# Optimization experiments

Measured on AMD Instinct MI355X. Metric: run time of the kernel, lower is better.

The kernel has to match this reference:

```python
import jax, jax.numpy as jnp
import numpy as np

N = 50000      # nodes
E = 500000     # edges
D_IN = 64      # node_in_dim
K = 4          # edge_in_dim
H = 64         # node_hidden_dim
C = 40         # num_class
L = 2          # num_layers


def setup_inputs() -> dict:
    key = jax.random.key(0)
    ks = jax.random.split(key, 10)
    node_features = jax.random.normal(ks[0], (N, D_IN), jnp.float32)
    edge_features = jax.random.normal(ks[1], (L, E, K), jnp.float32)
    src = jax.random.randint(ks[2], (E,), 0, N)
    dst = jax.random.randint(ks[3], (E,), 0, N)
    W0 = jax.random.normal(ks[4], (K * D_IN, H), jnp.float32) * 0.05
    b0 = jnp.zeros((H,), jnp.float32)
    W1 = jax.random.normal(ks[5], (K * H, H), jnp.float32) * 0.05
    b1 = jnp.zeros((H,), jnp.float32)
    Wfc = jax.random.normal(ks[6], (H, C), jnp.float32) * 0.05
    bfc = jnp.zeros((C,), jnp.float32)
    return dict(node_features=node_features, edge_features=edge_features,
                src=src, dst=dst, W0=W0, b0=b0, W1=W1, b1=b1, Wfc=Wfc, bfc=bfc)


def reference(node_features, edge_features, src, dst, W0, b0, W1, b1, Wfc, bfc):
    h = node_features  # [N, d]
    ones = jnp.ones((E,), jnp.float32)
    cnt = jnp.maximum(jax.ops.segment_sum(ones, dst, num_segments=N), 1.0)  # in-degree
    for i, (W, b) in enumerate([(W0, b0), (W1, b1)]):
        e = edge_features[i]          # [E, K]
        hs = h[src]                   # [E, d] edge gather of src node features
        d = hs.shape[1]
        # message: relu(Linear(flatten(e[:,:,None] * h[:,None,:])))
        # flatten order is (K, d), so reshape W -> [K, d, H] and contract directly
        Wr = W.reshape(K, d, H)
        m = jax.nn.relu(jnp.einsum('ek,ed,kdh->eh', e, hs, Wr) + b)  # [E, H]
        s = jax.ops.segment_sum(m, dst, num_segments=N)              # scatter-sum
        h = jax.nn.relu(s / cnt[:, None])                            # mailbox mean + relu
    return h @ Wfc + bfc  # [N, C]
```

## Files before the change

### kernel.cpp

```cpp
#include <hip/hip_runtime.h>
#include <hip/hip_fp16.h>

#define N_NODES 50000
#define N_EDGES 500000
#define DIM 64
#define KDIM 4
#define HID 64
#define NCLS 40
#define NBLK ((N_NODES + 255) / 256)

__device__ inline unsigned pack2(float a, float b) {
    __half2 h = __floats2half2_rn(a, b);
    return *(unsigned*)&h;
}
__device__ inline float2 unpack2(unsigned u) {
    __half2 h = *(__half2*)&u;
    return __half22float2(h);
}

__global__ void hist_k(const int* __restrict__ dst, int* __restrict__ cnt) {
    int e = blockIdx.x * 256 + threadIdx.x;
    if (e < N_EDGES) atomicAdd(&cnt[dst[e]], 1);
}

__global__ __launch_bounds__(256) void scan_k(const int* __restrict__ cnt,
                                              int* __restrict__ start,
                                              int* __restrict__ cursor,
                                              volatile int* __restrict__ bflag,
                                              volatile int* __restrict__ bval) {
    __shared__ int ls[256];
    __shared__ int sbase;
    __shared__ int ok_all;
    int b = blockIdx.x, t = threadIdx.x;
    int n = b * 256 + t;
    int v = (n < N_NODES) ? cnt[n] : 0;
    ls[t] = v;
    __syncthreads();
#pragma unroll
    for (int off = 1; off < 256; off <<= 1) {
        int u = (t >= off) ? ls[t - off] : 0;
        __syncthreads();
        ls[t] += u;
        __syncthreads();
    }
    int incl = ls[t];
    int total = ls[255];
    __syncthreads();

    if (t == 0) {
        bval[b] = total;
        __threadfence();
        bflag[b] = 1;
    }

    if (b > 0) {
        for (;;) {
            int f = (t < b) ? bflag[t] : 1;
            if (t == 0) ok_all = 1;
            __syncthreads();
            if (!f) ok_all = 0;
            __syncthreads();
            if (ok_all) break;
        }
        __threadfence();
        int pv = (t < b) ? bval[t] : 0;
        ls[t] = pv;
        __syncthreads();
#pragma unroll
        for (int off = 128; off > 0; off >>= 1) {
            if (t < off) ls[t] += ls[t + off];
            __syncthreads();
        }
        if (t == 0) sbase = ls[0];
        __syncthreads();
    } else {
        if (t == 0) sbase = 0;
        __syncthreads();
    }

    int excl = sbase + incl - v;
    if (n < N_NODES) { start[n] = excl; cursor[n] = excl; }
    if (n == 0) start[N_NODES] = N_EDGES;
}

__global__ void scatter_k(const int* __restrict__ src, const int* __restrict__ dst,
                          const float* __restrict__ ef, int* __restrict__ cursor,
                          uint4* __restrict__ rec) {
    int e = blockIdx.x * 256 + threadIdx.x;
    if (e < N_EDGES) {
        int d = dst[e];
        int pos = atomicAdd(&cursor[d], 1);
        int sn = src[e];
        float4 f0 = ((const float4*)ef)[e];
        float4 f1 = ((const float4*)ef)[N_EDGES + e];
        rec[2 * pos]     = make_uint4((unsigned)sn, pack2(f0.x, f0.y), pack2(f0.z, f0.w), 0u);
        rec[2 * pos + 1] = make_uint4((unsigned)sn, pack2(f1.x, f1.y), pack2(f1.z, f1.w), 0u);
    }
}

__global__ __launch_bounds__(256) void transform_k(const float* __restrict__ hin,
                                                   const float* __restrict__ W,
                                                   unsigned* __restrict__ y) {
    __shared__ float sW[2 * 64 * 64];
    __shared__ float sh[64 * 65];
    int t = threadIdx.x;
    int kpair = blockIdx.y;

    const float4* W4 = (const float4*)(W + (size_t)kpair * 2 * 4096);
    float4* sW4 = (float4*)sW;
#pragma unroll
    for (int i = 0; i < 8; ++i) sW4[t + 256 * i] = W4[t + 256 * i];

    int n0 = blockIdx.x * 64;
#pragma unroll
    for (int i = 0; i < 4; ++i) {
        int idx = t + 256 * i;
        int nl = idx >> 4;
        int dg = idx & 15;
        int n = n0 + nl;
        float4 v = make_float4(0.f, 0.f, 0.f, 0.f);
        if (n < N_NODES) v = ((const float4*)hin)[(size_t)n * 16 + dg];
        sh[nl * 65 + dg * 4 + 0] = v.x;
        sh[nl * 65 + dg * 4 + 1] = v.y;
        sh[nl * 65 + dg * 4 + 2] = v.z;
        sh[nl * 65 + dg * 4 + 3] = v.w;
    }
    __syncthreads();

    int nl = t & 31;
    int cg = t >> 5;
    int k_local = cg >> 2;
    int hc0 = (cg & 3) * 16;

    float acc0[16], acc1[16];
#pragma unroll
    for (int j = 0; j < 16; ++j) { acc0[j] = 0.f; acc1[j] = 0.f; }

    for (int d = 0; d < 64; ++d) {
        float a0 = sh[nl * 65 + d];
        float a1 = sh[(nl + 32) * 65 + d];
        const float* wr = &sW[k_local * 4096 + d * 64 + hc0];
#pragma unroll
        for (int j = 0; j < 16; ++j) {
            float w = wr[j];
            acc0[j] = fmaf(a0, w, acc0[j]);
            acc1[j] = fmaf(a1, w, acc1[j]);
        }
    }

    int n_a = n0 + nl, n_b = n0 + nl + 32;
    int cbase = (kpair * 2 + k_local) * 64 + hc0;
    if (n_a < N_NODES) {
        uint4* o = (uint4*)(y + ((size_t)n_a * 256 + cbase) / 2);
        o[0] = make_uint4(pack2(acc0[0], acc0[1]), pack2(acc0[2], acc0[3]),
                          pack2(acc0[4], acc0[5]), pack2(acc0[6], acc0[7]));
        o[1] = make_uint4(pack2(acc0[8], acc0[9]), pack2(acc0[10], acc0[11]),
                          pack2(acc0[12], acc0[13]), pack2(acc0[14], acc0[15]));
    }
    if (n_b < N_NODES) {
        uint4* o = (uint4*)(y + ((size_t)n_b * 256 + cbase) / 2);
        o[0] = make_uint4(pack2(acc1[0], acc1[1]), pack2(acc1[2], acc1[3]),
                          pack2(acc1[4], acc1[5]), pack2(acc1[6], acc1[7]));
        o[1] = make_uint4(pack2(acc1[8], acc1[9]), pack2(acc1[10], acc1[11]),
                          pack2(acc1[12], acc1[13]), pack2(acc1[14], acc1[15]));
    }
}

__device__ inline void load_edge(const uint4 r, const unsigned* __restrict__ y,
                                 int lane, uint2& q0, uint2& q1, uint2& q2, uint2& q3) {
    int sn = (int)r.x;
    const uint2* yb = (const uint2*)(y + (size_t)sn * 128);
    q0 = yb[lane];
    q1 = yb[16 + lane];
    q2 = yb[32 + lane];
    q3 = yb[48 + lane];
}

__device__ inline void compute_edge(const uint4 r, uint2 q0, uint2 q1, uint2 q2, uint2 q3,
                                    const float4 bias, float4& acc) {
    float2 e01 = unpack2(r.y);
    float2 e23 = unpack2(r.z);
    float2 a0 = unpack2(q0.x), a1 = unpack2(q0.y);
    float2 b0 = unpack2(q1.x), b1 = unpack2(q1.y);
    float2 c0 = unpack2(q2.x), c1 = unpack2(q2.y);
    float2 d0 = unpack2(q3.x), d1 = unpack2(q3.y);

    float4 z = bias;
    z.x = fmaf(e01.x, a0.x, z.x); z.y = fmaf(e01.x, a0.y, z.y);
    z.z = fmaf(e01.x, a1.x, z.z); z.w = fmaf(e01.x, a1.y, z.w);
    z.x = fmaf(e01.y, b0.x, z.x); z.y = fmaf(e01.y, b0.y, z.y);
    z.z = fmaf(e01.y, b1.x, z.z); z.w = fmaf(e01.y, b1.y, z.w);
    z.x = fmaf(e23.x, c0.x, z.x); z.y = fmaf(e23.x, c0.y, z.y);
    z.z = fmaf(e23.x, c1.x, z.z); z.w = fmaf(e23.x, c1.y, z.w);
    z.x = fmaf(e23.y, d0.x, z.x); z.y = fmaf(e23.y, d0.y, z.y);
    z.z = fmaf(e23.y, d1.x, z.z); z.w = fmaf(e23.y, d1.y, z.w);

    acc.x += fmaxf(z.x, 0.f);
    acc.y += fmaxf(z.y, 0.f);
    acc.z += fmaxf(z.z, 0.f);
    acc.w += fmaxf(z.w, 0.f);
}

__device__ inline float4 agg_core(const uint4* __restrict__ rec2,
                                  const int* __restrict__ start,
                                  const int* __restrict__ cnt,
                                  const unsigned* __restrict__ y,
                                  const float* __restrict__ b,
                                  int g, int lane) {
    int s0 = start[g];
    int deg = cnt[g];
    int s1 = s0 + deg;

    float4 bias = ((const float4*)b)[lane];
    float4 acc = make_float4(0.f, 0.f, 0.f, 0.f);

    int i = s0;
    for (; i + 4 <= s1; i += 4) {
        uint4 r0 = rec2[2 * i + 0];
        uint4 r1 = rec2[2 * i + 2];
        uint4 r2 = rec2[2 * i + 4];
        uint4 r3 = rec2[2 * i + 6];
        uint2 a0, a1, a2, a3, b0, b1, b2, b3, c0, c1, c2, c3, d0, d1, d2, d3;
        load_edge(r0, y, lane, a0, a1, a2, a3);
        load_edge(r1, y, lane, b0, b1, b2, b3);
        load_edge(r2, y, lane, c0, c1, c2, c3);
        load_edge(r3, y, lane, d0, d1, d2, d3);
        compute_edge(r0, a0, a1, a2, a3, bias, acc);
        compute_edge(r1, b0, b1, b2, b3, bias, acc);
        compute_edge(r2, c0, c1, c2, c3, bias, acc);
        compute_edge(r3, d0, d1, d2, d3, bias, acc);
    }
    if (i + 2 <= s1) {
        uint4 r0 = rec2[2 * i + 0];
        uint4 r1 = rec2[2 * i + 2];
        uint2 a0, a1, a2, a3, b0, b1, b2, b3;
        load_edge(r0, y, lane, a0, a1, a2, a3);
        load_edge(r1, y, lane, b0, b1, b2, b3);
        compute_edge(r0, a0, a1, a2, a3, bias, acc);
        compute_edge(r1, b0, b1, b2, b3, bias, acc);
        i += 2;
    }
    if (i < s1) {
        uint4 r0 = rec2[2 * i];
        uint2 a0, a1, a2, a3;
        load_edge(r0, y, lane, a0, a1, a2, a3);
        compute_edge(r0, a0, a1, a2, a3, bias, acc);
    }

    float inv = 1.0f / (float)(deg > 1 ? deg : 1);
    float4 r;
    r.x = fmaxf(acc.x * inv, 0.f);
    r.y = fmaxf(acc.y * inv, 0.f);
    r.z = fmaxf(acc.z * inv, 0.f);
    r.w = fmaxf(acc.w * inv, 0.f);
    return r;
}

__global__ __launch_bounds__(256) void agg_k(const uint4* __restrict__ rec2,
                                             const int* __restrict__ start,
                                             const int* __restrict__ cnt,
                                             const unsigned* __restrict__ y,
                                             const float* __restrict__ b,
                                             float* __restrict__ hout) {
    int t = blockIdx.x * 256 + threadIdx.x;
    int g = t >> 4;
    int lane = t & 15;
    float4 r = agg_core(rec2, start, cnt, y, b, g, lane);
    ((float4*)hout)[(size_t)g * 16 + lane] = r;
}

__global__ __launch_bounds__(256) void agg_fc_k(const uint4* __restrict__ rec2,
                                                const int* __restrict__ start,
                                                const int* __restrict__ cnt,
                                                const unsigned* __restrict__ y,
                                                const float* __restrict__ b,
                                                const float* __restrict__ Wfc,
                                                const float* __restrict__ bfc,
                                                float* __restrict__ out) {
    __shared__ float sh_h[16 * 65];
    __shared__ float sWfcT[NCLS * 65];
    __shared__ float sbfc[NCLS];
    int t = threadIdx.x;

    for (int i = t; i < 64 * NCLS; i += 256) {
        int j = i / NCLS;
        int c = i - j * NCLS;
        sWfcT[c * 65 + j] = Wfc[i];
    }
    if (t < NCLS) sbfc[t] = bfc[t];

    int nl = t >> 4;
    int lane = t & 15;
    int g = blockIdx.x * 16 + nl;

    float4 r = agg_core(rec2, start, cnt, y, b, g, lane);
    sh_h[nl * 65 + lane * 4 + 0] = r.x;
    sh_h[nl * 65 + lane * 4 + 1] = r.y;
    sh_h[nl * 65 + lane * 4 + 2] = r.z;
    sh_h[nl * 65 + lane * 4 + 3] = r.w;
    __syncthreads();

    for (int item = t; item < 16 * NCLS; item += 256) {
        int rn = item / NCLS;
        int c = item - rn * NCLS;
        float acc = sbfc[c];
        const float* hr = &sh_h[rn * 65];
        const float* wc = &sWfcT[c * 65];
#pragma unroll
        for (int j = 0; j < 64; ++j) acc = fmaf(hr[j], wc[j], acc);
        out[(size_t)(blockIdx.x * 16 + rn) * NCLS + c] = acc;
    }
}

extern "C" void kernel_launch(void* const* d_in, const int* in_sizes, int n_in,
                              void* d_out, int out_size, void* d_ws, size_t ws_size,
                              hipStream_t stream) {
    const float* nf  = (const float*)d_in[0];
    const float* ef  = (const float*)d_in[1];
    const int*   src = (const int*)d_in[2];
    const int*   dst = (const int*)d_in[3];
    const float* W0  = (const float*)d_in[4];
    const float* b0  = (const float*)d_in[5];
    const float* W1  = (const float*)d_in[6];
    const float* b1  = (const float*)d_in[7];
    const float* Wfc = (const float*)d_in[8];
    const float* bfc = (const float*)d_in[9];
    float* out = (float*)d_out;

    char* ws = (char*)d_ws;
    size_t off = 0;
    auto alloc = [&](size_t bytes) -> void* {
        void* p = ws + off;
        off = (off + bytes + 255) & ~(size_t)255;
        return p;
    };
    int*      zbuf   = (int*)     alloc((size_t)(50176 + 512) * 4);
    int*      cnt    = zbuf;
    int*      bflag  = zbuf + 50176;
    int*      bval   = zbuf + 50176 + 256;
    int*      start  = (int*)     alloc((size_t)(N_NODES + 1) * 4);
    int*      cursor = (int*)     alloc((size_t)N_NODES * 4);
    uint4*    rec    = (uint4*)   alloc((size_t)N_EDGES * 32);
    unsigned* y      = (unsigned*)alloc((size_t)N_NODES * 256 * 2);
    float*    hbuf   = (float*)   alloc((size_t)N_NODES * 64 * 4);

    hipMemsetAsync(zbuf, 0, (size_t)(50176 + 512) * 4, stream);

    hist_k<<<(N_EDGES + 255) / 256, 256, 0, stream>>>(dst, cnt);
    scan_k<<<NBLK, 256, 0, stream>>>(cnt, start, cursor, bflag, bval);
    scatter_k<<<(N_EDGES + 255) / 256, 256, 0, stream>>>(src, dst, ef, cursor, rec);

    dim3 tgrid((N_NODES + 63) / 64, 2);
    int agrid = N_NODES / 16;

    transform_k<<<tgrid, 256, 0, stream>>>(nf, W0, y);
    agg_k<<<agrid, 256, 0, stream>>>(rec, start, cnt, y, b0, hbuf);

    transform_k<<<tgrid, 256, 0, stream>>>(hbuf, W1, y);
    agg_fc_k<<<agrid, 256, 0, stream>>>(rec + 1, start, cnt, y, b1, Wfc, bfc, out);
}
```

Measured before the change: 299.7 us.

## Fuse node transform with source-ordered message computation into a per-edge message buffer

Builds a second CSR grouped by source node alongside the existing destination CSR. A fused kernel computes each node's transformed features into LDS, then computes messages for all its outgoing edges and writes them as fp32 rows into a message buffer indexed by destination slot. Separate aggregation kernels then read contiguous message rows and take the segment mean. This removes the random gather of transformed source features, but adds a 128 MB message buffer that is written and read each layer, plus a second histogram and scan with extra atomics.

```diff
diff --git a/kernel.cpp b/kernel.cpp
--- a/kernel.cpp
+++ b/kernel.cpp
@@ -3,11 +3,9 @@
 
 #define N_NODES 50000
 #define N_EDGES 500000
-#define DIM 64
-#define KDIM 4
-#define HID 64
 #define NCLS 40
 #define NBLK ((N_NODES + 255) / 256)
+#define EBLK ((N_EDGES + 255) / 256)
 
 __device__ inline unsigned pack2(float a, float b) {
     __half2 h = __floats2half2_rn(a, b);
@@ -18,9 +16,13 @@
     return __half22float2(h);
 }
 
-__global__ void hist_k(const int* __restrict__ dst, int* __restrict__ cnt) {
+__global__ void hist2_k(const int* __restrict__ src, const int* __restrict__ dst,
+                        int* __restrict__ cntD, int* __restrict__ cntS) {
     int e = blockIdx.x * 256 + threadIdx.x;
-    if (e < N_EDGES) atomicAdd(&cnt[dst[e]], 1);
+    if (e < N_EDGES) {
+        atomicAdd(&cntD[dst[e]], 1);
+        atomicAdd(&cntS[src[e]], 1);
+    }
 }
 
 __global__ __launch_bounds__(256) void scan_k(const int* __restrict__ cnt,
@@ -84,107 +86,27 @@
 }
 
 __global__ void scatter_k(const int* __restrict__ src, const int* __restrict__ dst,
-                          const float* __restrict__ ef, int* __restrict__ cursor,
-                          uint4* __restrict__ rec) {
+                          const float* __restrict__ ef,
+                          int* __restrict__ cursorD, int* __restrict__ cursorS,
+                          uint4* __restrict__ recS0, uint4* __restrict__ recS1) {
     int e = blockIdx.x * 256 + threadIdx.x;
     if (e < N_EDGES) {
-        int d = dst[e];
-        int pos = atomicAdd(&cursor[d], 1);
-        int sn = src[e];
+        int d = dst[e], s = src[e];
+        int pD = atomicAdd(&cursorD[d], 1);
+        int pS = atomicAdd(&cursorS[s], 1);
         float4 f0 = ((const float4*)ef)[e];
         float4 f1 = ((const float4*)ef)[N_EDGES + e];
-        rec[2 * pos]     = make_uint4((unsigned)sn, pack2(f0.x, f0.y), pack2(f0.z, f0.w), 0u);
-        rec[2 * pos + 1] = make_uint4((unsigned)sn, pack2(f1.x, f1.y), pack2(f1.z, f1.w), 0u);
-    }
-}
-
-__global__ __launch_bounds__(256) void transform_k(const float* __restrict__ hin,
-                                                   const float* __restrict__ W,
-                                                   unsigned* __restrict__ y) {
-    __shared__ float sW[2 * 64 * 64];
-    __shared__ float sh[64 * 65];
-    int t = threadIdx.x;
-    int kpair = blockIdx.y;
-
-    const float4* W4 = (const float4*)(W + (size_t)kpair * 2 * 4096);
-    float4* sW4 = (float4*)sW;
-#pragma unroll
-    for (int i = 0; i < 8; ++i) sW4[t + 256 * i] = W4[t + 256 * i];
-
-    int n0 = blockIdx.x * 64;
-#pragma unroll
-    for (int i = 0; i < 4; ++i) {
-        int idx = t + 256 * i;
-        int nl = idx >> 4;
-        int dg = idx & 15;
-        int n = n0 + nl;
-        float4 v = make_float4(0.f, 0.f, 0.f, 0.f);
-        if (n < N_NODES) v = ((const float4*)hin)[(size_t)n * 16 + dg];
-        sh[nl * 65 + dg * 4 + 0] = v.x;
-        sh[nl * 65 + dg * 4 + 1] = v.y;
-        sh[nl * 65 + dg * 4 + 2] = v.z;
-        sh[nl * 65 + dg * 4 + 3] = v.w;
-    }
-    __syncthreads();
-
-    int nl = t & 31;
-    int cg = t >> 5;
-    int k_local = cg >> 2;
-    int hc0 = (cg & 3) * 16;
-
-    float acc0[16], acc1[16];
-#pragma unroll
-    for (int j = 0; j < 16; ++j) { acc0[j] = 0.f; acc1[j] = 0.f; }
-
-    for (int d = 0; d < 64; ++d) {
-        float a0 = sh[nl * 65 + d];
-        float a1 = sh[(nl + 32) * 65 + d];
-        const float* wr = &sW[k_local * 4096 + d * 64 + hc0];
-#pragma unroll
-        for (int j = 0; j < 16; ++j) {
-            float w = wr[j];
-            acc0[j] = fmaf(a0, w, acc0[j]);
-            acc1[j] = fmaf(a1, w, acc1[j]);
-        }
-    }
-
-    int n_a = n0 + nl, n_b = n0 + nl + 32;
-    int cbase = (kpair * 2 + k_local) * 64 + hc0;
-    if (n_a < N_NODES) {
-        uint4* o = (uint4*)(y + ((size_t)n_a * 256 + cbase) / 2);
-        o[0] = make_uint4(pack2(acc0[0], acc0[1]), pack2(acc0[2], acc0[3]),
-                          pack2(acc0[4], acc0[5]), pack2(acc0[6], acc0[7]));
-        o[1] = make_uint4(pack2(acc0[8], acc0[9]), pack2(acc0[10], acc0[11]),
-                          pack2(acc0[12], acc0[13]), pack2(acc0[14], acc0[15]));
-    }
-    if (n_b < N_NODES) {
-        uint4* o = (uint4*)(y + ((size_t)n_b * 256 + cbase) / 2);
-        o[0] = make_uint4(pack2(acc1[0], acc1[1]), pack2(acc1[2], acc1[3]),
-                          pack2(acc1[4], acc1[5]), pack2(acc1[6], acc1[7]));
-        o[1] = make_uint4(pack2(acc1[8], acc1[9]), pack2(acc1[10], acc1[11]),
-                          pack2(acc1[12], acc1[13]), pack2(acc1[14], acc1[15]));
-    }
-}
-
-__device__ inline void load_edge(const uint4 r, const unsigned* __restrict__ y,
-                                 int lane, uint2& q0, uint2& q1, uint2& q2, uint2& q3) {
-    int sn = (int)r.x;
-    const uint2* yb = (const uint2*)(y + (size_t)sn * 128);
-    q0 = yb[lane];
-    q1 = yb[16 + lane];
-    q2 = yb[32 + lane];
-    q3 = yb[48 + lane];
-}
-
-__device__ inline void compute_edge(const uint4 r, uint2 q0, uint2 q1, uint2 q2, uint2 q3,
-                                    const float4 bias, float4& acc) {
-    float2 e01 = unpack2(r.y);
-    float2 e23 = unpack2(r.z);
-    float2 a0 = unpack2(q0.x), a1 = unpack2(q0.y);
-    float2 b0 = unpack2(q1.x), b1 = unpack2(q1.y);
-    float2 c0 = unpack2(q2.x), c1 = unpack2(q2.y);
-    float2 d0 = unpack2(q3.x), d1 = unpack2(q3.y);
-
+        recS0[pS] = make_uint4((unsigned)pD, pack2(f0.x, f0.y), pack2(f0.z, f0.w), 0u);
+        recS1[pS] = make_uint4((unsigned)pD, pack2(f1.x, f1.y), pack2(f1.z, f1.w), 0u);
+    }
+}
+
+__device__ inline float4 msg_from(uint4 rec,
+                                  float2 a0, float2 a1, float2 b0, float2 b1,
+                                  float2 c0, float2 c1, float2 d0, float2 d1,
+                                  float4 bias) {
+    float2 e01 = unpack2(rec.y);
+    float2 e23 = unpack2(rec.z);
     float4 z = bias;
     z.x = fmaf(e01.x, a0.x, z.x); z.y = fmaf(e01.x, a0.y, z.y);
     z.z = fmaf(e01.x, a1.x, z.z); z.w = fmaf(e01.x, a1.y, z.w);
@@ -194,86 +116,151 @@
     z.z = fmaf(e23.x, c1.x, z.z); z.w = fmaf(e23.x, c1.y, z.w);
     z.x = fmaf(e23.y, d0.x, z.x); z.y = fmaf(e23.y, d0.y, z.y);
     z.z = fmaf(e23.y, d1.x, z.z); z.w = fmaf(e23.y, d1.y, z.w);
-
-    acc.x += fmaxf(z.x, 0.f);
-    acc.y += fmaxf(z.y, 0.f);
-    acc.z += fmaxf(z.z, 0.f);
-    acc.w += fmaxf(z.w, 0.f);
-}
-
-__device__ inline float4 agg_core(const uint4* __restrict__ rec2,
-                                  const int* __restrict__ start,
-                                  const int* __restrict__ cnt,
-                                  const unsigned* __restrict__ y,
-                                  const float* __restrict__ b,
-                                  int g, int lane) {
-    int s0 = start[g];
-    int deg = cnt[g];
-    int s1 = s0 + deg;
-
+    z.x = fmaxf(z.x, 0.f); z.y = fmaxf(z.y, 0.f);
+    z.z = fmaxf(z.z, 0.f); z.w = fmaxf(z.w, 0.f);
+    return z;
+}
+
+__global__ __launch_bounds__(256) void fused_k(const float* __restrict__ hin,
+                                               const float* __restrict__ W,
+                                               const float* __restrict__ b,
+                                               const uint4* __restrict__ recS,
+                                               const int* __restrict__ startS,
+                                               const int* __restrict__ cntS,
+                                               float* __restrict__ mbuf) {
+    __shared__ float shT[64 * 64];
+    __shared__ float sW[64 * 64];
+    __shared__ unsigned yL[64 * 128];
+    int t = threadIdx.x;
+    int n0 = blockIdx.x * 64;
+
+#pragma unroll
+    for (int i = 0; i < 4; ++i) {
+        int idx = t + 256 * i;
+        int nl = idx >> 4;
+        int dg = idx & 15;
+        int n = n0 + nl;
+        float4 v = make_float4(0.f, 0.f, 0.f, 0.f);
+        if (n < N_NODES) v = ((const float4*)hin)[(size_t)n * 16 + dg];
+        shT[(dg * 4 + 0) * 64 + nl] = v.x;
+        shT[(dg * 4 + 1) * 64 + nl] = v.y;
+        shT[(dg * 4 + 2) * 64 + nl] = v.z;
+        shT[(dg * 4 + 3) * 64 + nl] = v.w;
+    }
+
+    int nl2 = t & 31;
+    int cg = t >> 5;
+    int hc0 = cg * 8;
+    for (int k = 0; k < 4; ++k) {
+        const float4* W4 = (const float4*)(W + (size_t)k * 4096);
+        float4* sW4 = (float4*)sW;
+#pragma unroll
+        for (int i = 0; i < 4; ++i) sW4[t + 256 * i] = W4[t + 256 * i];
+        __syncthreads();
+        float acc0[8], acc1[8];
+#pragma unroll
+        for (int j = 0; j < 8; ++j) { acc0[j] = 0.f; acc1[j] = 0.f; }
+        for (int d = 0; d < 64; ++d) {
+            float a0 = shT[d * 64 + nl2];
+            float a1 = shT[d * 64 + nl2 + 32];
+            const float4* wr4 = (const float4*)&sW[d * 64 + hc0];
+            float4 wa = wr4[0], wb = wr4[1];
+            acc0[0] = fmaf(a0, wa.x, acc0[0]); acc1[0] = fmaf(a1, wa.x, acc1[0]);
+            acc0[1] = fmaf(a0, wa.y, acc0[1]); acc1[1] = fmaf(a1, wa.y, acc1[1]);
+            acc0[2] = fmaf(a0, wa.z, acc0[2]); acc1[2] = fmaf(a1, wa.z, acc1[2]);
+            acc0[3] = fmaf(a0, wa.w, acc0[3]); acc1[3] = fmaf(a1, wa.w, acc1[3]);
+            acc0[4] = fmaf(a0, wb.x, acc0[4]); acc1[4] = fmaf(a1, wb.x, acc1[4]);
+            acc0[5] = fmaf(a0, wb.y, acc0[5]); acc1[5] = fmaf(a1, wb.y, acc1[5]);
+            acc0[6] = fmaf(a0, wb.z, acc0[6]); acc1[6] = fmaf(a1, wb.z, acc1[6]);
+            acc0[7] = fmaf(a0, wb.w, acc0[7]); acc1[7] = fmaf(a1, wb.w, acc1[7]);
+        }
+        unsigned* y0 = &yL[nl2 * 128 + k * 32 + cg * 4];
+        unsigned* y1 = &yL[(nl2 + 32) * 128 + k * 32 + cg * 4];
+#pragma unroll
+        for (int j = 0; j < 4; ++j) {
+            y0[j] = pack2(acc0[2 * j], acc0[2 * j + 1]);
+            y1[j] = pack2(acc1[2 * j], acc1[2 * j + 1]);
+        }
+        __syncthreads();
+    }
+
+    int gi = t >> 4;
+    int lane = t & 15;
     float4 bias = ((const float4*)b)[lane];
-    float4 acc = make_float4(0.f, 0.f, 0.f, 0.f);
-
-    int i = s0;
-    for (; i + 4 <= s1; i += 4) {
-        uint4 r0 = rec2[2 * i + 0];
-        uint4 r1 = rec2[2 * i + 2];
-        uint4 r2 = rec2[2 * i + 4];
-        uint4 r3 = rec2[2 * i + 6];
-        uint2 a0, a1, a2, a3, b0, b1, b2, b3, c0, c1, c2, c3, d0, d1, d2, d3;
-        load_edge(r0, y, lane, a0, a1, a2, a3);
-        load_edge(r1, y, lane, b0, b1, b2, b3);
-        load_edge(r2, y, lane, c0, c1, c2, c3);
-        load_edge(r3, y, lane, d0, d1, d2, d3);
-        compute_edge(r0, a0, a1, a2, a3, bias, acc);
-        compute_edge(r1, b0, b1, b2, b3, bias, acc);
-        compute_edge(r2, c0, c1, c2, c3, bias, acc);
-        compute_edge(r3, d0, d1, d2, d3, bias, acc);
-    }
-    if (i + 2 <= s1) {
-        uint4 r0 = rec2[2 * i + 0];
-        uint4 r1 = rec2[2 * i + 2];
-        uint2 a0, a1, a2, a3, b0, b1, b2, b3;
-        load_edge(r0, y, lane, a0, a1, a2, a3);
-        load_edge(r1, y, lane, b0, b1, b2, b3);
-        compute_edge(r0, a0, a1, a2, a3, bias, acc);
-        compute_edge(r1, b0, b1, b2, b3, bias, acc);
-        i += 2;
-    }
-    if (i < s1) {
-        uint4 r0 = rec2[2 * i];
-        uint2 a0, a1, a2, a3;
-        load_edge(r0, y, lane, a0, a1, a2, a3);
-        compute_edge(r0, a0, a1, a2, a3, bias, acc);
-    }
-
-    float inv = 1.0f / (float)(deg > 1 ? deg : 1);
+    float4* mb4 = (float4*)mbuf;
+    for (int r = 0; r < 4; ++r) {
+        int nl = r * 16 + gi;
+        int n = n0 + nl;
+        if (n >= N_NODES) continue;
+        const unsigned* yr = &yL[nl * 128];
+        uint2 q0 = *(const uint2*)&yr[0 * 32 + 2 * lane];
+        uint2 q1 = *(const uint2*)&yr[1 * 32 + 2 * lane];
+        uint2 q2 = *(const uint2*)&yr[2 * 32 + 2 * lane];
+        uint2 q3 = *(const uint2*)&yr[3 * 32 + 2 * lane];
+        float2 a0 = unpack2(q0.x), a1 = unpack2(q0.y);
+        float2 b0 = unpack2(q1.x), b1 = unpack2(q1.y);
+        float2 c0 = unpack2(q2.x), c1 = unpack2(q2.y);
+        float2 d0 = unpack2(q3.x), d1 = unpack2(q3.y);
+        int sS = startS[n], cS = cntS[n];
+        int i = 0;
+        for (; i + 2 <= cS; i += 2) {
+            uint4 rA = recS[sS + i];
+            uint4 rB = recS[sS + i + 1];
+            float4 mA = msg_from(rA, a0, a1, b0, b1, c0, c1, d0, d1, bias);
+            float4 mB = msg_from(rB, a0, a1, b0, b1, c0, c1, d0, d1, bias);
+            mb4[(size_t)rA.x * 16 + lane] = mA;
+            mb4[(size_t)rB.x * 16 + lane] = mB;
+        }
+        if (i < cS) {
+            uint4 rA = recS[sS + i];
+            mb4[(size_t)rA.x * 16 + lane] = msg_from(rA, a0, a1, b0, b1, c0, c1, d0, d1, bias);
+        }
+    }
+}
+
+__device__ inline float4 seg_mean_relu(const float* __restrict__ mbuf,
+                                       int s0, int c, int lane) {
+    const float4* mb = (const float4*)mbuf + (size_t)s0 * 16 + lane;
+    float4 p0 = make_float4(0.f, 0.f, 0.f, 0.f);
+    float4 p1 = p0, p2 = p0, p3 = p0;
+    int i = 0;
+    for (; i + 4 <= c; i += 4) {
+        float4 v0 = mb[(size_t)(i + 0) * 16];
+        float4 v1 = mb[(size_t)(i + 1) * 16];
+        float4 v2 = mb[(size_t)(i + 2) * 16];
+        float4 v3 = mb[(size_t)(i + 3) * 16];
+        p0.x += v0.x; p0.y += v0.y; p0.z += v0.z; p0.w += v0.w;
+        p1.x += v1.x; p1.y += v1.y; p1.z += v1.z; p1.w += v1.w;
+        p2.x += v2.x; p2.y += v2.y; p2.z += v2.z; p2.w += v2.w;
+        p3.x += v3.x; p3.y += v3.y; p3.z += v3.z; p3.w += v3.w;
+    }
+    for (; i < c; ++i) {
+        float4 v = mb[(size_t)i * 16];
+        p0.x += v.x; p0.y += v.y; p0.z += v.z; p0.w += v.w;
+    }
+    float inv = 1.0f / (float)(c > 1 ? c : 1);
     float4 r;
-    r.x = fmaxf(acc.x * inv, 0.f);
-    r.y = fmaxf(acc.y * inv, 0.f);
-    r.z = fmaxf(acc.z * inv, 0.f);
-    r.w = fmaxf(acc.w * inv, 0.f);
+    r.x = fmaxf((p0.x + p1.x + p2.x + p3.x) * inv, 0.f);
+    r.y = fmaxf((p0.y + p1.y + p2.y + p3.y) * inv, 0.f);
+    r.z = fmaxf((p0.z + p1.z + p2.z + p3.z) * inv, 0.f);
+    r.w = fmaxf((p0.w + p1.w + p2.w + p3.w) * inv, 0.f);
     return r;
 }
 
-__global__ __launch_bounds__(256) void agg_k(const uint4* __restrict__ rec2,
-                                             const int* __restrict__ start,
-                                             const int* __restrict__ cnt,
-                                             const unsigned* __restrict__ y,
-                                             const float* __restrict__ b,
+__global__ __launch_bounds__(256) void agg_k(const float* __restrict__ mbuf,
+                                             const int* __restrict__ startD,
+                                             const int* __restrict__ cntD,
                                              float* __restrict__ hout) {
     int t = blockIdx.x * 256 + threadIdx.x;
     int g = t >> 4;
     int lane = t & 15;
-    float4 r = agg_core(rec2, start, cnt, y, b, g, lane);
+    float4 r = seg_mean_relu(mbuf, startD[g], cntD[g], lane);
     ((float4*)hout)[(size_t)g * 16 + lane] = r;
 }
 
-__global__ __launch_bounds__(256) void agg_fc_k(const uint4* __restrict__ rec2,
-                                                const int* __restrict__ start,
-                                                const int* __restrict__ cnt,
-                                                const unsigned* __restrict__ y,
-                                                const float* __restrict__ b,
+__global__ __launch_bounds__(256) void agg_fc_k(const float* __restrict__ mbuf,
+                                                const int* __restrict__ startD,
+                                                const int* __restrict__ cntD,
                                                 const float* __restrict__ Wfc,
                                                 const float* __restrict__ bfc,
                                                 float* __restrict__ out) {
@@ -293,7 +280,7 @@
     int lane = t & 15;
     int g = blockIdx.x * 16 + nl;
 
-    float4 r = agg_core(rec2, start, cnt, y, b, g, lane);
+    float4 r = seg_mean_relu(mbuf, startD[g], cntD[g], lane);
     sh_h[nl * 65 + lane * 4 + 0] = r.x;
     sh_h[nl * 65 + lane * 4 + 1] = r.y;
     sh_h[nl * 65 + lane * 4 + 2] = r.z;
@@ -334,28 +321,35 @@
         off = (off + bytes + 255) & ~(size_t)255;
         return p;
     };
-    int*      zbuf   = (int*)     alloc((size_t)(50176 + 512) * 4);
-    int*      cnt    = zbuf;
-    int*      bflag  = zbuf + 50176;
-    int*      bval   = zbuf + 50176 + 256;
-    int*      start  = (int*)     alloc((size_t)(N_NODES + 1) * 4);
-    int*      cursor = (int*)     alloc((size_t)N_NODES * 4);
-    uint4*    rec    = (uint4*)   alloc((size_t)N_EDGES * 32);
-    unsigned* y      = (unsigned*)alloc((size_t)N_NODES * 256 * 2);
-    float*    hbuf   = (float*)   alloc((size_t)N_NODES * 64 * 4);
-
-    hipMemsetAsync(zbuf, 0, (size_t)(50176 + 512) * 4, stream);
-
-    hist_k<<<(N_EDGES + 255) / 256, 256, 0, stream>>>(dst, cnt);
-    scan_k<<<NBLK, 256, 0, stream>>>(cnt, start, cursor, bflag, bval);
-    scatter_k<<<(N_EDGES + 255) / 256, 256, 0, stream>>>(src, dst, ef, cursor, rec);
-
-    dim3 tgrid((N_NODES + 63) / 64, 2);
+    int* zbuf    = (int*)alloc((size_t)(2 * 50176 + 1024) * 4);
+    int* cntD    = zbuf;
+    int* cntS    = zbuf + 50176;
+    int* bflagD  = zbuf + 2 * 50176;
+    int* bvalD   = bflagD + 256;
+    int* bflagS  = bvalD + 256;
+    int* bvalS   = bflagS + 256;
+    int* startD  = (int*)alloc((size_t)(N_NODES + 4) * 4);
+    int* cursorD = (int*)alloc((size_t)N_NODES * 4);
+    int* startS  = (int*)alloc((size_t)(N_NODES + 4) * 4);
+    int* cursorS = (int*)alloc((size_t)N_NODES * 4);
+    uint4* recS0 = (uint4*)alloc((size_t)N_EDGES * 16);
+    uint4* recS1 = (uint4*)alloc((size_t)N_EDGES * 16);
+    float* mbuf  = (float*)alloc((size_t)N_EDGES * 64 * 4);
+    float* hbuf  = (float*)alloc((size_t)N_NODES * 64 * 4);
+
+    hipMemsetAsync(zbuf, 0, (size_t)(2 * 50176 + 1024) * 4, stream);
+
+    hist2_k<<<EBLK, 256, 0, stream>>>(src, dst, cntD, cntS);
+    scan_k<<<NBLK, 256, 0, stream>>>(cntD, startD, cursorD, bflagD, bvalD);
+    scan_k<<<NBLK, 256, 0, stream>>>(cntS, startS, cursorS, bflagS, bvalS);
+    scatter_k<<<EBLK, 256, 0, stream>>>(src, dst, ef, cursorD, cursorS, recS0, recS1);
+
+    int fgrid = (N_NODES + 63) / 64;
     int agrid = N_NODES / 16;
 
-    transform_k<<<tgrid, 256, 0, stream>>>(nf, W0, y);
-    agg_k<<<agrid, 256, 0, stream>>>(rec, start, cnt, y, b0, hbuf);
-
-    transform_k<<<tgrid, 256, 0, stream>>>(hbuf, W1, y);
-    agg_fc_k<<<agrid, 256, 0, stream>>>(rec + 1, start, cnt, y, b1, Wfc, bfc, out);
-}
+    fused_k<<<fgrid, 256, 0, stream>>>(nf, W0, b0, recS0, startS, cntS, mbuf);
+    agg_k<<<agrid, 256, 0, stream>>>(mbuf, startD, cntD, hbuf);
+
+    fused_k<<<fgrid, 256, 0, stream>>>(hbuf, W1, b1, recS1, startS, cntS, mbuf);
+    agg_fc_k<<<agrid, 256, 0, stream>>>(mbuf, startD, cntD, Wfc, bfc, out);
+}
```

Measured after the change: 411.9 us. 1.37x slower.

## Interleave transformed node features by K and use nontemporal edge record access

Applied to the files above, without the earlier changes.

The per-node transformed feature table is relaid out so that each output column's four K-slices sit next to each other. Each lane in the aggregation can then fetch its data with two 16-byte loads per edge instead of four 8-byte loads, and each lane now owns hidden columns 2*lane, 2*lane+1, 32+2*lane and 33+2*lane. The transform kernel is restructured to compute both k-slices of a pair per thread, matching the new write pattern. Edge records are written and read with nontemporal hints so they do not evict the reused node feature table from cache. The tradeoff is that the transform writes become scattered 8-byte stores rather than contiguous 16-byte ones.

```diff
diff --git a/kernel.cpp b/kernel.cpp
--- a/kernel.cpp
+++ b/kernel.cpp
@@ -8,6 +8,9 @@
 #define HID 64
 #define NCLS 40
 #define NBLK ((N_NODES + 255) / 256)
+#define EBLK ((N_EDGES + 255) / 256)
+
+typedef unsigned uv4 __attribute__((ext_vector_type(4)));
 
 __device__ inline unsigned pack2(float a, float b) {
     __half2 h = __floats2half2_rn(a, b);
@@ -16,6 +19,14 @@
 __device__ inline float2 unpack2(unsigned u) {
     __half2 h = *(__half2*)&u;
     return __half22float2(h);
+}
+__device__ inline uint4 ldnt4(const uint4* p) {
+    uv4 v = __builtin_nontemporal_load((const uv4*)p);
+    return make_uint4(v.x, v.y, v.z, v.w);
+}
+__device__ inline void stnt4(uint4* p, uint4 v) {
+    uv4 w = {v.x, v.y, v.z, v.w};
+    __builtin_nontemporal_store(w, (uv4*)p);
 }
 
 __global__ void hist_k(const int* __restrict__ dst, int* __restrict__ cnt) {
@@ -93,8 +104,8 @@
         int sn = src[e];
         float4 f0 = ((const float4*)ef)[e];
         float4 f1 = ((const float4*)ef)[N_EDGES + e];
-        rec[2 * pos]     = make_uint4((unsigned)sn, pack2(f0.x, f0.y), pack2(f0.z, f0.w), 0u);
-        rec[2 * pos + 1] = make_uint4((unsigned)sn, pack2(f1.x, f1.y), pack2(f1.z, f1.w), 0u);
+        stnt4(&rec[2 * pos],     make_uint4((unsigned)sn, pack2(f0.x, f0.y), pack2(f0.z, f0.w), 0u));
+        stnt4(&rec[2 * pos + 1], make_uint4((unsigned)sn, pack2(f1.x, f1.y), pack2(f1.z, f1.w), 0u));
     }
 }
 
@@ -104,9 +115,9 @@
     __shared__ float sW[2 * 64 * 64];
     __shared__ float sh[64 * 65];
     int t = threadIdx.x;
-    int kpair = blockIdx.y;
-
-    const float4* W4 = (const float4*)(W + (size_t)kpair * 2 * 4096);
+    int kp = blockIdx.y;
+
+    const float4* W4 = (const float4*)(W + (size_t)kp * 2 * 4096);
     float4* sW4 = (float4*)sW;
 #pragma unroll
     for (int i = 0; i < 8; ++i) sW4[t + 256 * i] = W4[t + 256 * i];
@@ -129,76 +140,89 @@
 
     int nl = t & 31;
     int cg = t >> 5;
-    int k_local = cg >> 2;
-    int hc0 = (cg & 3) * 16;
-
-    float acc0[16], acc1[16];
-#pragma unroll
-    for (int j = 0; j < 16; ++j) { acc0[j] = 0.f; acc1[j] = 0.f; }
+    int j0 = cg * 8;
+
+    float a0c[8][2], a1c[8][2];
+#pragma unroll
+    for (int c = 0; c < 8; ++c) {
+        a0c[c][0] = 0.f; a0c[c][1] = 0.f;
+        a1c[c][0] = 0.f; a1c[c][1] = 0.f;
+    }
 
     for (int d = 0; d < 64; ++d) {
         float a0 = sh[nl * 65 + d];
         float a1 = sh[(nl + 32) * 65 + d];
-        const float* wr = &sW[k_local * 4096 + d * 64 + hc0];
-#pragma unroll
-        for (int j = 0; j < 16; ++j) {
-            float w = wr[j];
-            acc0[j] = fmaf(a0, w, acc0[j]);
-            acc1[j] = fmaf(a1, w, acc1[j]);
-        }
-    }
-
-    int n_a = n0 + nl, n_b = n0 + nl + 32;
-    int cbase = (kpair * 2 + k_local) * 64 + hc0;
-    if (n_a < N_NODES) {
-        uint4* o = (uint4*)(y + ((size_t)n_a * 256 + cbase) / 2);
-        o[0] = make_uint4(pack2(acc0[0], acc0[1]), pack2(acc0[2], acc0[3]),
-                          pack2(acc0[4], acc0[5]), pack2(acc0[6], acc0[7]));
-        o[1] = make_uint4(pack2(acc0[8], acc0[9]), pack2(acc0[10], acc0[11]),
-                          pack2(acc0[12], acc0[13]), pack2(acc0[14], acc0[15]));
-    }
-    if (n_b < N_NODES) {
-        uint4* o = (uint4*)(y + ((size_t)n_b * 256 + cbase) / 2);
-        o[0] = make_uint4(pack2(acc1[0], acc1[1]), pack2(acc1[2], acc1[3]),
-                          pack2(acc1[4], acc1[5]), pack2(acc1[6], acc1[7]));
-        o[1] = make_uint4(pack2(acc1[8], acc1[9]), pack2(acc1[10], acc1[11]),
-                          pack2(acc1[12], acc1[13]), pack2(acc1[14], acc1[15]));
+        const float4* wl = (const float4*)&sW[d * 64 + j0];
+        const float4* wh = (const float4*)&sW[4096 + d * 64 + j0];
+        float4 wl0 = wl[0], wl1 = wl[1];
+        float4 wh0 = wh[0], wh1 = wh[1];
+        float wlv[8] = {wl0.x, wl0.y, wl0.z, wl0.w, wl1.x, wl1.y, wl1.z, wl1.w};
+        float whv[8] = {wh0.x, wh0.y, wh0.z, wh0.w, wh1.x, wh1.y, wh1.z, wh1.w};
+#pragma unroll
+        for (int c = 0; c < 8; ++c) {
+            a0c[c][0] = fmaf(a0, wlv[c], a0c[c][0]);
+            a0c[c][1] = fmaf(a0, whv[c], a0c[c][1]);
+            a1c[c][0] = fmaf(a1, wlv[c], a1c[c][0]);
+            a1c[c][1] = fmaf(a1, whv[c], a1c[c][1]);
+        }
+    }
+
+    int blk = cg >> 2;
+    int l0 = (cg & 3) * 4;
+    int nA = n0 + nl, nB = n0 + nl + 32;
+    if (nA < N_NODES) {
+        unsigned* yb = y + (size_t)nA * 128 + blk * 64 + kp * 2;
+#pragma unroll
+        for (int i2 = 0; i2 < 4; ++i2) {
+            uint2 v2 = make_uint2(pack2(a0c[2 * i2][0],     a0c[2 * i2][1]),
+                                  pack2(a0c[2 * i2 + 1][0], a0c[2 * i2 + 1][1]));
+            *(uint2*)(yb + (l0 + i2) * 4) = v2;
+        }
+    }
+    if (nB < N_NODES) {
+        unsigned* yb = y + (size_t)nB * 128 + blk * 64 + kp * 2;
+#pragma unroll
+        for (int i2 = 0; i2 < 4; ++i2) {
+            uint2 v2 = make_uint2(pack2(a1c[2 * i2][0],     a1c[2 * i2][1]),
+                                  pack2(a1c[2 * i2 + 1][0], a1c[2 * i2 + 1][1]));
+            *(uint2*)(yb + (l0 + i2) * 4) = v2;
+        }
     }
 }
 
 __device__ inline void load_edge(const uint4 r, const unsigned* __restrict__ y,
-                                 int lane, uint2& q0, uint2& q1, uint2& q2, uint2& q3) {
-    int sn = (int)r.x;
-    const uint2* yb = (const uint2*)(y + (size_t)sn * 128);
-    q0 = yb[lane];
-    q1 = yb[16 + lane];
-    q2 = yb[32 + lane];
-    q3 = yb[48 + lane];
-}
-
-__device__ inline void compute_edge(const uint4 r, uint2 q0, uint2 q1, uint2 q2, uint2 q3,
+                                 int lane, uint4& qlo, uint4& qhi) {
+    const uint4* yb = (const uint4*)(y + (size_t)r.x * 128);
+    qlo = yb[lane];
+    qhi = yb[16 + lane];
+}
+
+__device__ inline void compute_edge(const uint4 r, uint4 qlo, uint4 qhi,
                                     const float4 bias, float4& acc) {
     float2 e01 = unpack2(r.y);
     float2 e23 = unpack2(r.z);
-    float2 a0 = unpack2(q0.x), a1 = unpack2(q0.y);
-    float2 b0 = unpack2(q1.x), b1 = unpack2(q1.y);
-    float2 c0 = unpack2(q2.x), c1 = unpack2(q2.y);
-    float2 d0 = unpack2(q3.x), d1 = unpack2(q3.y);
-
-    float4 z = bias;
-    z.x = fmaf(e01.x, a0.x, z.x); z.y = fmaf(e01.x, a0.y, z.y);
-    z.z = fmaf(e01.x, a1.x, z.z); z.w = fmaf(e01.x, a1.y, z.w);
-    z.x = fmaf(e01.y, b0.x, z.x); z.y = fmaf(e01.y, b0.y, z.y);
-    z.z = fmaf(e01.y, b1.x, z.z); z.w = fmaf(e01.y, b1.y, z.w);
-    z.x = fmaf(e23.x, c0.x, z.x); z.y = fmaf(e23.x, c0.y, z.y);
-    z.z = fmaf(e23.x, c1.x, z.z); z.w = fmaf(e23.x, c1.y, z.w);
-    z.x = fmaf(e23.y, d0.x, z.x); z.y = fmaf(e23.y, d0.y, z.y);
-    z.z = fmaf(e23.y, d1.x, z.z); z.w = fmaf(e23.y, d1.y, z.w);
-
-    acc.x += fmaxf(z.x, 0.f);
-    acc.y += fmaxf(z.y, 0.f);
-    acc.z += fmaxf(z.z, 0.f);
-    acc.w += fmaxf(z.w, 0.f);
+    float2 p, q;
+    float z;
+    p = unpack2(qlo.x); q = unpack2(qlo.z);
+    z = bias.x;
+    z = fmaf(e01.x, p.x, z); z = fmaf(e01.y, p.y, z);
+    z = fmaf(e23.x, q.x, z); z = fmaf(e23.y, q.y, z);
+    acc.x += fmaxf(z, 0.f);
+    p = unpack2(qlo.y); q = unpack2(qlo.w);
+    z = bias.y;
+    z = fmaf(e01.x, p.x, z); z = fmaf(e01.y, p.y, z);
+    z = fmaf(e23.x, q.x, z); z = fmaf(e23.y, q.y, z);
+    acc.y += fmaxf(z, 0.f);
+    p = unpack2(qhi.x); q = unpack2(qhi.z);
+    z = bias.z;
+    z = fmaf(e01.x, p.x, z); z = fmaf(e01.y, p.y, z);
+    z = fmaf(e23.x, q.x, z); z = fmaf(e23.y, q.y, z);
+    acc.z += fmaxf(z, 0.f);
+    p = unpack2(qhi.y); q = unpack2(qhi.w);
+    z = bias.w;
+    z = fmaf(e01.x, p.x, z); z = fmaf(e01.y, p.y, z);
+    z = fmaf(e23.x, q.x, z); z = fmaf(e23.y, q.y, z);
+    acc.w += fmaxf(z, 0.f);
 }
 
 __device__ inline float4 agg_core(const uint4* __restrict__ rec2,
@@ -211,40 +235,42 @@
     int deg = cnt[g];
     int s1 = s0 + deg;
 
-    float4 bias = ((const float4*)b)[lane];
+    float2 blo = ((const float2*)b)[lane];
+    float2 bhi = ((const float2*)b)[16 + lane];
+    float4 bias = make_float4(blo.x, blo.y, bhi.x, bhi.y);
     float4 acc = make_float4(0.f, 0.f, 0.f, 0.f);
 
     int i = s0;
     for (; i + 4 <= s1; i += 4) {
-        uint4 r0 = rec2[2 * i + 0];
-        uint4 r1 = rec2[2 * i + 2];
-        uint4 r2 = rec2[2 * i + 4];
-        uint4 r3 = rec2[2 * i + 6];
-        uint2 a0, a1, a2, a3, b0, b1, b2, b3, c0, c1, c2, c3, d0, d1, d2, d3;
-        load_edge(r0, y, lane, a0, a1, a2, a3);
-        load_edge(r1, y, lane, b0, b1, b2, b3);
-        load_edge(r2, y, lane, c0, c1, c2, c3);
-        load_edge(r3, y, lane, d0, d1, d2, d3);
-        compute_edge(r0, a0, a1, a2, a3, bias, acc);
-        compute_edge(r1, b0, b1, b2, b3, bias, acc);
-        compute_edge(r2, c0, c1, c2, c3, bias, acc);
-        compute_edge(r3, d0, d1, d2, d3, bias, acc);
+        uint4 r0 = ldnt4(&rec2[2 * i + 0]);
+        uint4 r1 = ldnt4(&rec2[2 * i + 2]);
+        uint4 r2 = ldnt4(&rec2[2 * i + 4]);
+        uint4 r3 = ldnt4(&rec2[2 * i + 6]);
+        uint4 aL, aH, bL, bH, cL, cH, dL, dH;
+        load_edge(r0, y, lane, aL, aH);
+        load_edge(r1, y, lane, bL, bH);
+        load_edge(r2, y, lane, cL, cH);
+        load_edge(r3, y, lane, dL, dH);
+        compute_edge(r0, aL, aH, bias, acc);
+        compute_edge(r1, bL, bH, bias, acc);
+        compute_edge(r2, cL, cH, bias, acc);
+        compute_edge(r3, dL, dH, bias, acc);
     }
     if (i + 2 <= s1) {
-        uint4 r0 = rec2[2 * i + 0];
-        uint4 r1 = rec2[2 * i + 2];
-        uint2 a0, a1, a2, a3, b0, b1, b2, b3;
-        load_edge(r0, y, lane, a0, a1, a2, a3);
-        load_edge(r1, y, lane, b0, b1, b2, b3);
-        compute_edge(r0, a0, a1, a2, a3, bias, acc);
-        compute_edge(r1, b0, b1, b2, b3, bias, acc);
+        uint4 r0 = ldnt4(&rec2[2 * i + 0]);
+        uint4 r1 = ldnt4(&rec2[2 * i + 2]);
+        uint4 aL, aH, bL, bH;
+        load_edge(r0, y, lane, aL, aH);
+        load_edge(r1, y, lane, bL, bH);
+        compute_edge(r0, aL, aH, bias, acc);
+        compute_edge(r1, bL, bH, bias, acc);
         i += 2;
     }
     if (i < s1) {
-        uint4 r0 = rec2[2 * i];
-        uint2 a0, a1, a2, a3;
-        load_edge(r0, y, lane, a0, a1, a2, a3);
-        compute_edge(r0, a0, a1, a2, a3, bias, acc);
+        uint4 r0 = ldnt4(&rec2[2 * i]);
+        uint4 aL, aH;
+        load_edge(r0, y, lane, aL, aH);
+        compute_edge(r0, aL, aH, bias, acc);
     }
 
     float inv = 1.0f / (float)(deg > 1 ? deg : 1);
@@ -266,7 +292,9 @@
     int g = t >> 4;
     int lane = t & 15;
     float4 r = agg_core(rec2, start, cnt, y, b, g, lane);
-    ((float4*)hout)[(size_t)g * 16 + lane] = r;
+    float2* o = (float2*)(hout + (size_t)g * 64);
+    o[lane]      = make_float2(r.x, r.y);
+    o[16 + lane] = make_float2(r.z, r.w);
 }
 
 __global__ __launch_bounds__(256) void agg_fc_k(const uint4* __restrict__ rec2,
@@ -294,10 +322,10 @@
     int g = blockIdx.x * 16 + nl;
 
     float4 r = agg_core(rec2, start, cnt, y, b, g, lane);
-    sh_h[nl * 65 + lane * 4 + 0] = r.x;
-    sh_h[nl * 65 + lane * 4 + 1] = r.y;
-    sh_h[nl * 65 + lane * 4 + 2] = r.z;
-    sh_h[nl * 65 + lane * 4 + 3] = r.w;
+    sh_h[nl * 65 + 2 * lane]      = r.x;
+    sh_h[nl * 65 + 2 * lane + 1]  = r.y;
+    sh_h[nl * 65 + 32 + 2 * lane] = r.z;
+    sh_h[nl * 65 + 33 + 2 * lane] = r.w;
     __syncthreads();
 
     for (int item = t; item < 16 * NCLS; item += 256) {
@@ -346,9 +374,9 @@
 
     hipMemsetAsync(zbuf, 0, (size_t)(50176 + 512) * 4, stream);
 
-    hist_k<<<(N_EDGES + 255) / 256, 256, 0, stream>>>(dst, cnt);
+    hist_k<<<EBLK, 256, 0, stream>>>(dst, cnt);
     scan_k<<<NBLK, 256, 0, stream>>>(cnt, start, cursor, bflag, bval);
-    scatter_k<<<(N_EDGES + 255) / 256, 256, 0, stream>>>(src, dst, ef, cursor, rec);
+    scatter_k<<<EBLK, 256, 0, stream>>>(src, dst, ef, cursor, rec);
 
     dim3 tgrid((N_NODES + 63) / 64, 2);
     int agrid = N_NODES / 16;
```

Measured after the change: 330.9 us. +10.4%, slower.
